# Kernel tuning notes

Hardware: AMD Instinct MI355X
Metric: run time of the kernel (lower is better)

## Reference

```python
import jax, jax.numpy as jnp
import numpy as np

B, C, H, W = 16, 512, 64, 64
HEADS = 8
DIL = 2  # dilation of the 3x3 depthwise conv (padding == dilation -> shape preserving)


def setup_inputs() -> dict:
    key = jax.random.key(0)
    ks = jax.random.split(key, 4)
    x = jax.random.normal(ks[0], (B, C, H, W), jnp.float32)
    # kaiming-normal-ish scales (fan_out, relu)
    w_qkv = jax.random.normal(ks[1], (3 * C, C), jnp.float32) * (2.0 / C) ** 0.5  # 1x1 conv weight
    w_dw = jax.random.normal(ks[2], (C, 3, 3), jnp.float32) * (2.0 / 9.0) ** 0.5  # depthwise 3x3
    w_out = jax.random.normal(ks[3], (C, C), jnp.float32) * (2.0 / C) ** 0.5      # 1x1 conv weight
    temperature = jnp.sqrt(jnp.asarray(C // HEADS, jnp.float32))                  # init sqrt(dim_per_head)
    return {"x": x, "w_qkv": w_qkv, "w_dw": w_dw, "w_out": w_out, "temperature": temperature}


def _dw_conv(y, w_dw):
    # depthwise dilated 3x3 conv, padding=dilation -> same spatial size
    rhs = w_dw[:, None, :, :]  # [C,1,3,3]
    return jax.lax.conv_general_dilated(
        y, rhs, window_strides=(1, 1), padding=((DIL, DIL), (DIL, DIL)),
        rhs_dilation=(DIL, DIL), feature_group_count=y.shape[1],
        dimension_numbers=("NCHW", "OIHW", "NCHW"))


def reference(x, w_qkv, w_dw, w_out, temperature):
    b, c, h, w = x.shape
    n = h * w
    d = c // HEADS
    # 1x1 qkv projection (bias-free conv == einsum)
    qkv = jnp.einsum("oc,bchw->bohw", w_qkv, x)  # [B,3C,H,W]
    q, k, v = jnp.split(qkv, 3, axis=1)
    # same depthwise conv applied to q,k,v: fold into batch, conv once
    qkv3 = _dw_conv(jnp.concatenate([q, k, v], axis=0), w_dw)  # [3B,C,H,W]
    q, k, v = jnp.split(qkv3, 3, axis=0)
    q = q.reshape(b, HEADS, d, n)
    k = k.reshape(b, HEADS, d, n)
    v = v.reshape(b, HEADS, d, n)
    # L2 normalize along the per-head channel dim (dim=2), eps=1e-12 like F.normalize
    l2 = lambda t: t / jnp.maximum(jnp.linalg.norm(t, axis=2, keepdims=True), 1e-12)
    q = l2(q)
    k = l2(k)
    # cross-covariance attention: [B,heads,d,d]
    attn = jnp.einsum("bhdn,bhen->bhde", q, k) / jnp.maximum(temperature, 1e-5)
    attn = jax.nn.softmax(attn, axis=-1)
    # dropout is identity in eval mode
    out = jnp.einsum("bhde,bhen->bhdn", attn, v).reshape(b, c, h, w)
    return jnp.einsum("oc,bchw->bohw", w_out, out)
```

## Files before the change

### kernel.cpp

```cpp
#include <hip/hip_runtime.h>

typedef __attribute__((ext_vector_type(8))) short bf16x8;
typedef __attribute__((ext_vector_type(8))) unsigned short ushort8;
typedef __attribute__((ext_vector_type(4))) float f32x4;
typedef __attribute__((ext_vector_type(2))) float f32x2;
typedef __attribute__((ext_vector_type(4))) unsigned int u32x4;
typedef __attribute__((ext_vector_type(2))) unsigned int u32x2;

__device__ __forceinline__ float bf2f(unsigned short u) {
  union { unsigned int i; float f; } v; v.i = ((unsigned int)u) << 16; return v.f;
}
__device__ __forceinline__ float asf(unsigned int u) {
  union { unsigned int i; float f; } v; v.i = u; return v.f;
}
__device__ __forceinline__ unsigned short f2bf(float f) {
  union { float f; unsigned int i; } v; v.f = f;
  unsigned int u = v.i;
  return (unsigned short)((u + 0x7FFFu + ((u >> 16) & 1u)) >> 16);
}
__device__ __forceinline__ void gload16(const void* g, void* l) {
  __builtin_amdgcn_global_load_lds(
      (const __attribute__((address_space(1))) void*)g,
      (__attribute__((address_space(3))) void*)l, 16, 0, 0);
}

__global__ __launch_bounds__(256) void cvt_f32_bf16(const float* __restrict__ s,
                                                    unsigned short* __restrict__ d, int n) {
  int i = blockIdx.x * 256 + threadIdx.x;
  if (i < n) d[i] = f2bf(s[i]);
}

__global__ __launch_bounds__(256) void transpose_x(const float* __restrict__ x,
                                                   unsigned short* __restrict__ xt) {
  __shared__ float tile[64][65];
  const int b = blockIdx.z, ct = blockIdx.y, nt = blockIdx.x;
  const int t = threadIdx.x;
  const int r0 = t >> 6, col = t & 63;
  const float* src = x + ((size_t)b * 512 + ct * 64) * 4096 + nt * 64;
#pragma unroll
  for (int i = 0; i < 16; ++i) {
    int r = i * 4 + r0;
    tile[r][col] = src[(size_t)r * 4096 + col];
  }
  __syncthreads();
  unsigned short* dst = xt + ((size_t)b * 4096 + nt * 64) * 512 + ct * 64;
  const int c2 = (t & 31) * 2;
  const int nsub = t >> 5;
#pragma unroll
  for (int i = 0; i < 8; ++i) {
    int n = i * 8 + nsub;
    unsigned int p;
    asm("v_cvt_pk_bf16_f32 %0, %1, %2" : "=v"(p) : "v"(tile[c2][n]), "v"(tile[c2 + 1][n]));
    *(unsigned int*)(dst + (size_t)n * 512 + c2) = p;
  }
}

template <bool BF16OUT>
__global__ __launch_bounds__(512, 1) void gemm256_8ph(const unsigned short* __restrict__ A,
                                                      const unsigned short* __restrict__ B,
                                                      void* __restrict__ Cv, int ldc,
                                                      size_t sA, size_t sB, size_t sC) {
  __shared__ unsigned short lA[2][256 * 64];
  __shared__ unsigned short lB[2][256 * 64];
  const int gx = gridDim.x, gy = gridDim.y;
  const int nwg = gx * gy * gridDim.z;
  int flat = blockIdx.x + gx * (blockIdx.y + gy * blockIdx.z);
  flat = (flat & 7) * (nwg >> 3) + (flat >> 3);
  const int bx = flat % gx;
  const int rem = flat / gx;
  const int by = rem % gy;
  const int bz = rem / gy;
  const size_t m0 = (size_t)by * 256;
  const size_t n0 = (size_t)bx * 256;
  A += (size_t)bz * sA;
  B += (size_t)bz * sB;

  const int t = threadIdx.x;
  const int lane = t & 63;
  const int wid = t >> 6;
  const int wm = wid >> 2, wn = wid & 3;
  const int ro = lane & 15, kq = lane >> 4;

  const int srow = t >> 3;
  const int sslot = t & 7;
  const int kslot = sslot ^ (srow & 7);

  auto stageA = [&](int kt, int h, int bbuf) {
    char* d = (char*)(&lA[bbuf][0]) + ((h * 128 + srow) * 64 + sslot * 8) * 2;
    const unsigned short* g = A + (m0 + h * 128 + srow) * 512 + kt * 64 + kslot * 8;
    gload16(g, d);
    gload16(g + (size_t)64 * 512, d + 64 * 128);
  };
  auto stageB = [&](int kt, int h, int bbuf) {
    char* d = (char*)(&lB[bbuf][0]) + ((h * 128 + srow) * 64 + sslot * 8) * 2;
    const unsigned short* g = B + (n0 + h * 128 + srow) * 512 + kt * 64 + kslot * 8;
    gload16(g, d);
    gload16(g + (size_t)64 * 512, d + 64 * 128);
  };

  f32x4 acc[8][4] = {};

  stageA(0, 0, 0); stageA(0, 1, 0);
  stageB(0, 0, 0); stageB(0, 1, 0);
  stageA(1, 0, 1); stageA(1, 1, 1);
  asm volatile("s_waitcnt vmcnt(4)" ::: "memory");
  __builtin_amdgcn_s_barrier();

#pragma unroll 1
  for (int kt = 0; kt < 8; ++kt) {
    const int c = kt & 1;
    const unsigned short* pa = &lA[c][0];
    const unsigned short* pb = &lB[c][0];
    const int slot0 = kq ^ (ro & 7);
    const int slot1 = (4 + kq) ^ (ro & 7);

    bf16x8 a0[8], a1[8], b0, b1, b2, b3;
#pragma unroll
    for (int i = 0; i < 8; ++i)
      a0[i] = *(const bf16x8*)&pa[(wm * 128 + i * 16 + ro) * 64 + slot0 * 8];
    b0 = *(const bf16x8*)&pb[(wn * 64 + 0 * 16 + ro) * 64 + slot0 * 8];
    b1 = *(const bf16x8*)&pb[(wn * 64 + 1 * 16 + ro) * 64 + slot0 * 8];
    if (kt + 1 < 8) stageB(kt + 1, 0, c ^ 1);
    asm volatile("" ::: "memory");
    __builtin_amdgcn_s_barrier();
    asm volatile("s_waitcnt lgkmcnt(0)" ::: "memory");
    __builtin_amdgcn_s_setprio(1);
#pragma unroll
    for (int i = 0; i < 8; ++i) {
      acc[i][0] = __builtin_amdgcn_mfma_f32_16x16x32_bf16(a0[i], b0, acc[i][0], 0, 0, 0);
      acc[i][1] = __builtin_amdgcn_mfma_f32_16x16x32_bf16(a0[i], b1, acc[i][1], 0, 0, 0);
    }
    __builtin_amdgcn_s_setprio(0);

    b2 = *(const bf16x8*)&pb[(wn * 64 + 2 * 16 + ro) * 64 + slot0 * 8];
    b3 = *(const bf16x8*)&pb[(wn * 64 + 3 * 16 + ro) * 64 + slot0 * 8];
    if (kt + 1 < 8) stageB(kt + 1, 1, c ^ 1);
    asm volatile("" ::: "memory");
    __builtin_amdgcn_s_barrier();
    asm volatile("s_waitcnt lgkmcnt(0)" ::: "memory");
    __builtin_amdgcn_s_setprio(1);
#pragma unroll
    for (int i = 0; i < 8; ++i) {
      acc[i][2] = __builtin_amdgcn_mfma_f32_16x16x32_bf16(a0[i], b2, acc[i][2], 0, 0, 0);
      acc[i][3] = __builtin_amdgcn_mfma_f32_16x16x32_bf16(a0[i], b3, acc[i][3], 0, 0, 0);
    }
    __builtin_amdgcn_s_setprio(0);

#pragma unroll
    for (int i = 0; i < 8; ++i)
      a1[i] = *(const bf16x8*)&pa[(wm * 128 + i * 16 + ro) * 64 + slot1 * 8];
    b0 = *(const bf16x8*)&pb[(wn * 64 + 0 * 16 + ro) * 64 + slot1 * 8];
    b1 = *(const bf16x8*)&pb[(wn * 64 + 1 * 16 + ro) * 64 + slot1 * 8];
    asm volatile("s_waitcnt lgkmcnt(0)" ::: "memory");
    __builtin_amdgcn_s_barrier();
    __builtin_amdgcn_s_setprio(1);
#pragma unroll
    for (int i = 0; i < 8; ++i) {
      acc[i][0] = __builtin_amdgcn_mfma_f32_16x16x32_bf16(a1[i], b0, acc[i][0], 0, 0, 0);
      acc[i][1] = __builtin_amdgcn_mfma_f32_16x16x32_bf16(a1[i], b1, acc[i][1], 0, 0, 0);
    }
    __builtin_amdgcn_s_setprio(0);

    b2 = *(const bf16x8*)&pb[(wn * 64 + 2 * 16 + ro) * 64 + slot1 * 8];
    b3 = *(const bf16x8*)&pb[(wn * 64 + 3 * 16 + ro) * 64 + slot1 * 8];
    if (kt + 2 < 8) { stageA(kt + 2, 0, c); stageA(kt + 2, 1, c); }
    asm volatile("s_waitcnt lgkmcnt(0)" ::: "memory");
    if (kt < 6)       asm volatile("s_waitcnt vmcnt(4)" ::: "memory");
    else if (kt == 6) asm volatile("s_waitcnt vmcnt(0)" ::: "memory");
    __builtin_amdgcn_s_barrier();
    __builtin_amdgcn_s_setprio(1);
#pragma unroll
    for (int i = 0; i < 8; ++i) {
      acc[i][2] = __builtin_amdgcn_mfma_f32_16x16x32_bf16(a1[i], b2, acc[i][2], 0, 0, 0);
      acc[i][3] = __builtin_amdgcn_mfma_f32_16x16x32_bf16(a1[i], b3, acc[i][3], 0, 0, 0);
    }
    __builtin_amdgcn_s_setprio(0);
  }

  if constexpr (BF16OUT) {
    unsigned short* C = (unsigned short*)Cv;
#pragma unroll
    for (int i = 0; i < 8; ++i)
#pragma unroll
      for (int j = 0; j < 4; ++j)
#pragma unroll
        for (int r = 0; r < 4; ++r) {
          size_t row = m0 + wm * 128 + i * 16 + (kq << 2) + r;
          size_t col = n0 + wn * 64 + j * 16 + ro;
          C[row * (size_t)ldc + col] = f2bf(acc[i][j][r]);
        }
  } else {
    float* C = (float*)Cv + (size_t)bz * sC;
#pragma unroll
    for (int i = 0; i < 8; ++i)
#pragma unroll
      for (int j = 0; j < 4; ++j)
#pragma unroll
        for (int r = 0; r < 4; ++r) {
          size_t row = m0 + wm * 128 + i * 16 + (kq << 2) + r;
          size_t col = n0 + wn * 64 + j * 16 + ro;
          C[row * (size_t)ldc + col] = acc[i][j][r];
        }
  }
}

struct Row4 { u32x2 v[4]; };

__global__ __launch_bounds__(256) void dwconv_norm(const unsigned short* __restrict__ Y,
                                                   const float* __restrict__ wdw,
                                                   unsigned short* __restrict__ Qb,
                                                   unsigned short* __restrict__ Kb,
                                                   unsigned short* __restrict__ Vb) {
  const int t = threadIdx.x, lane = t & 63, wv = t >> 6;
  const int bid = blockIdx.x;
  const int lbid = (bid & 7) * 384 + (bid >> 3);
  const int wid = lbid * 4 + wv;
  const int sub = wid & 255;
  const int grp = wid >> 8;
  const int pair = sub >> 3;
  const int par = (sub >> 2) & 1, chhalf = (sub >> 1) & 1, rowhalf = sub & 1;
  const int b = grp / 3, part = grp - b * 3;
  const int x0 = (pair >> 1) * 4 + (pair & 1);
  const int c0 = chhalf * 256 + (lane >> 4) * 64 + (lane & 15) * 4;

  f32x2 wa[9], wb[9];
  {
    float qw[36];
    const float* wp = wdw + c0 * 9;
#pragma unroll
    for (int i = 0; i < 9; ++i) {
      f32x4 q = *(const f32x4*)(wp + i * 4);
      qw[i * 4 + 0] = q[0]; qw[i * 4 + 1] = q[1];
      qw[i * 4 + 2] = q[2]; qw[i * 4 + 3] = q[3];
    }
#pragma unroll
    for (int tap = 0; tap < 9; ++tap) {
      wa[tap] = (f32x2){qw[tap], qw[9 + tap]};
      wb[tap] = (f32x2){qw[18 + tap], qw[27 + tap]};
    }
  }

  const size_t ybase = (size_t)b * 4096 * 1536 + part * 512 + c0;
  const bool okm = (x0 >= 2), okp = (x0 + 4 <= 63);
  const int cm = okm ? x0 - 2 : x0;
  const int cp = okp ? x0 + 4 : x0;

  auto loadrow = [&](int yy) -> Row4 {
    Row4 r;
    const bool oky = ((unsigned)yy < 64u);
    const int yyc = oky ? yy : 0;
    const size_t rb = ybase + (size_t)(yyc * 64) * 1536;
    u32x2 a = *(const u32x2*)(Y + rb + (size_t)cm * 1536);
    u32x2 c = *(const u32x2*)(Y + rb + (size_t)x0 * 1536);
    u32x2 d = *(const u32x2*)(Y + rb + (size_t)(x0 + 2) * 1536);
    u32x2 e = *(const u32x2*)(Y + rb + (size_t)cp * 1536);
    r.v[0] = a & ((oky && okm) ? 0xFFFFFFFFu : 0u);
    r.v[1] = c & (oky ? 0xFFFFFFFFu : 0u);
    r.v[2] = d & (oky ? 0xFFFFFFFFu : 0u);
    r.v[3] = e & ((oky && okp) ? 0xFFFFFFFFu : 0u);
    return r;
  };

  const int y0 = par + rowhalf * 32;
  Row4 W[3];
  W[0] = loadrow(y0 - 2);
  W[1] = loadrow(y0);
  W[2] = loadrow(y0 + 2);

  unsigned short* dstA = (part == 0 ? Qb : (part == 1 ? Kb : Vb)) +
                         ((size_t)b * 4096 + x0) * 512 + c0;
  unsigned short* dstB = dstA + (size_t)2 * 512;

#pragma unroll
  for (int i = 0; i < 16; ++i) {
    const int y = y0 + 2 * i;
    f32x2 A01 = (f32x2){0.f, 0.f}, A23 = (f32x2){0.f, 0.f};
    f32x2 B01 = (f32x2){0.f, 0.f}, B23 = (f32x2){0.f, 0.f};
#pragma unroll
    for (int r = 0; r < 3; ++r) {
      const Row4& R = W[(i + r) % 3];
#pragma unroll
      for (int xt = 0; xt < 4; ++xt) {
        const u32x2 v = R.v[xt];
        f32x2 lo = (f32x2){asf(v[0] << 16), asf(v[0] & 0xFFFF0000u)};
        f32x2 hi = (f32x2){asf(v[1] << 16), asf(v[1] & 0xFFFF0000u)};
        if (xt < 3) {
          const int tap = r * 3 + xt;
          A01 += lo * wa[tap];
          A23 += hi * wb[tap];
        }
        if (xt >= 1) {
          const int tap = r * 3 + xt - 1;
          B01 += lo * wa[tap];
          B23 += hi * wb[tap];
        }
      }
    }
    if (part < 2) {
      f32x2 sa = A01 * A01 + A23 * A23;
      f32x2 sb = B01 * B01 + B23 * B23;
      float ssa = sa[0] + sa[1];
      float ssb = sb[0] + sb[1];
#pragma unroll
      for (int m = 1; m <= 8; m <<= 1) {
        ssa += __shfl_xor(ssa, m);
        ssb += __shfl_xor(ssb, m);
      }
      const float ra = 1.f / fmaxf(sqrtf(ssa), 1e-12f);
      const float rb2 = 1.f / fmaxf(sqrtf(ssb), 1e-12f);
      A01 *= ra; A23 *= ra;
      B01 *= rb2; B23 *= rb2;
    }
    unsigned int p0, p1, q0, q1;
    asm("v_cvt_pk_bf16_f32 %0, %1, %2" : "=v"(p0) : "v"(A01[0]), "v"(A01[1]));
    asm("v_cvt_pk_bf16_f32 %0, %1, %2" : "=v"(p1) : "v"(A23[0]), "v"(A23[1]));
    asm("v_cvt_pk_bf16_f32 %0, %1, %2" : "=v"(q0) : "v"(B01[0]), "v"(B01[1]));
    asm("v_cvt_pk_bf16_f32 %0, %1, %2" : "=v"(q1) : "v"(B23[0]), "v"(B23[1]));
    u32x2 pkA; pkA[0] = p0; pkA[1] = p1;
    u32x2 pkB; pkB[0] = q0; pkB[1] = q1;
    *(u32x2*)(dstA + (size_t)y * 64 * 512) = pkA;
    *(u32x2*)(dstB + (size_t)y * 64 * 512) = pkB;
    if (i < 15) W[i % 3] = loadrow(y + 4);
  }
}

__global__ __launch_bounds__(256) void attn_partial(const unsigned short* __restrict__ Qb,
                                                    const unsigned short* __restrict__ Kb,
                                                    float* __restrict__ Spart) {
  __shared__ unsigned short sQ[4][64][72];
  __shared__ unsigned short sK[4][64][72];
  const int t = threadIdx.x, lane = t & 63, wv = t >> 6;
  const int bh = blockIdx.x >> 2;
  const int s = (blockIdx.x & 3) * 4 + wv;
  const int b = bh >> 3, h = bh & 7;
  const unsigned short* qbase = Qb + ((size_t)b * 4096) * 512 + h * 64;
  const unsigned short* kbase = Kb + ((size_t)b * 4096) * 512 + h * 64;
  f32x4 acc[4][4] = {};
  for (int ch = 0; ch < 4; ++ch) {
    const int n0 = s * 256 + ch * 64;
    const unsigned short* qp = qbase + (size_t)(n0 + lane) * 512;
    const unsigned short* kp = kbase + (size_t)(n0 + lane) * 512;
    ushort8 qv[8], kv[8];
#pragma unroll
    for (int v = 0; v < 8; ++v) qv[v] = *(const ushort8*)(qp + v * 8);
#pragma unroll
    for (int v = 0; v < 8; ++v) kv[v] = *(const ushort8*)(kp + v * 8);
#pragma unroll
    for (int v = 0; v < 8; ++v)
#pragma unroll
      for (int j = 0; j < 8; ++j) {
        sQ[wv][v * 8 + j][lane] = qv[v][j];
        sK[wv][v * 8 + j][lane] = kv[v][j];
      }
    __syncthreads();
    const int ro = lane & 15, ko = (lane >> 4) * 8;
#pragma unroll
    for (int ks = 0; ks < 2; ++ks) {
      bf16x8 af[4], bv[4];
#pragma unroll
      for (int i = 0; i < 4; ++i) af[i] = *(const bf16x8*)&sQ[wv][i * 16 + ro][ks * 32 + ko];
#pragma unroll
      for (int i = 0; i < 4; ++i) bv[i] = *(const bf16x8*)&sK[wv][i * 16 + ro][ks * 32 + ko];
#pragma unroll
      for (int i = 0; i < 4; ++i)
#pragma unroll
        for (int j = 0; j < 4; ++j)
          acc[i][j] = __builtin_amdgcn_mfma_f32_16x16x32_bf16(af[i], bv[j], acc[i][j], 0, 0, 0);
    }
    __syncthreads();
  }
  float* dst = Spart + ((size_t)bh * 16 + s) * 4096;
#pragma unroll
  for (int i = 0; i < 4; ++i)
#pragma unroll
    for (int j = 0; j < 4; ++j)
#pragma unroll
      for (int r = 0; r < 4; ++r) {
        int d = i * 16 + ((lane >> 4) << 2) + r;
        int e = j * 16 + (lane & 15);
        dst[d * 64 + e] = acc[i][j][r];
      }
}

__global__ __launch_bounds__(256) void softmax_attn(const float* __restrict__ Spart,
                                                    const float* __restrict__ tptr,
                                                    unsigned short* __restrict__ attn) {
  const int bh = blockIdx.x, t = threadIdx.x;
  const int d = t >> 2, eb = (t & 3) << 4;
  const float inv_t = 1.f / fmaxf(tptr[0], 1e-5f);
  float v[16];
#pragma unroll
  for (int i = 0; i < 16; ++i) v[i] = 0.f;
  for (int s = 0; s < 16; ++s) {
    const f32x4* p = (const f32x4*)(Spart + ((size_t)bh * 16 + s) * 4096 + d * 64 + eb);
#pragma unroll
    for (int i = 0; i < 4; ++i) {
      f32x4 q = p[i];
      v[i * 4 + 0] += q[0]; v[i * 4 + 1] += q[1];
      v[i * 4 + 2] += q[2]; v[i * 4 + 3] += q[3];
    }
  }
  float mx = -1e30f;
#pragma unroll
  for (int i = 0; i < 16; ++i) { v[i] *= inv_t; mx = fmaxf(mx, v[i]); }
  mx = fmaxf(mx, __shfl_xor(mx, 1));
  mx = fmaxf(mx, __shfl_xor(mx, 2));
  float sm = 0.f;
#pragma unroll
  for (int i = 0; i < 16; ++i) { v[i] = __expf(v[i] - mx); sm += v[i]; }
  sm += __shfl_xor(sm, 1);
  sm += __shfl_xor(sm, 2);
  const float r = 1.f / sm;
  ushort8 pk0, pk1;
#pragma unroll
  for (int i = 0; i < 8; ++i) { pk0[i] = f2bf(v[i] * r); pk1[i] = f2bf(v[8 + i] * r); }
  ushort8* dst = (ushort8*)(attn + (size_t)bh * 4096 + d * 64 + eb);
  dst[0] = pk0; dst[1] = pk1;
}

__global__ __launch_bounds__(256) void make_w2(const unsigned short* __restrict__ attn,
                                               const float* __restrict__ w_out,
                                               unsigned short* __restrict__ w2) {
  __shared__ float sA[4096];
  const int bx = blockIdx.x;
  const int bh = bx >> 1, half = bx & 1;
  const int b = bh >> 3, h = bh & 7;
  const int t = threadIdx.x;
  for (int i = t; i < 4096; i += 256) sA[i] = bf2f(attn[(size_t)bh * 4096 + i]);
  __syncthreads();
  const int o = half * 256 + t;
  float w[64];
  const float* wp = w_out + (size_t)o * 512 + h * 64;
#pragma unroll
  for (int i = 0; i < 64; i += 4) {
    f32x4 q = *(const f32x4*)(wp + i);
    w[i] = q[0]; w[i + 1] = q[1]; w[i + 2] = q[2]; w[i + 3] = q[3];
  }
  unsigned short* dst = w2 + ((size_t)b * 512 + o) * 512 + h * 64;
#pragma unroll 1
  for (int eg = 0; eg < 8; ++eg) {
    ushort8 pk;
#pragma unroll
    for (int ee = 0; ee < 8; ++ee) {
      const int e = eg * 8 + ee;
      float acc = 0.f;
#pragma unroll
      for (int dd = 0; dd < 64; ++dd) acc += w[dd] * sA[dd * 64 + e];
      pk[ee] = f2bf(acc);
    }
    *(ushort8*)(dst + eg * 8) = pk;
  }
}

extern "C" void kernel_launch(void* const* d_in, const int* in_sizes, int n_in,
                              void* d_out, int out_size, void* d_ws, size_t ws_size,
                              hipStream_t stream) {
  const float* x     = (const float*)d_in[0];
  const float* w_qkv = (const float*)d_in[1];
  const float* w_dw  = (const float*)d_in[2];
  const float* w_out = (const float*)d_in[3];
  const float* temp  = (const float*)d_in[4];
  float* out = (float*)d_out;

  char* ws = (char*)d_ws;
  const size_t MB = 1024 * 1024;
  unsigned short* Xt    = (unsigned short*)(ws);
  float*          Spart = (float*)(ws);
  unsigned short* attn  = (unsigned short*)(ws + 32 * MB);
  unsigned short* w2    = (unsigned short*)(ws + 33 * MB);
  unsigned short* Y     = (unsigned short*)(ws + 64 * MB);
  unsigned short* Qb    = (unsigned short*)(ws + 256 * MB);
  unsigned short* Kb    = (unsigned short*)(ws + 320 * MB);
  unsigned short* Vb    = (unsigned short*)(ws + 384 * MB);
  unsigned short* Wq    = (unsigned short*)(ws + 448 * MB);

  cvt_f32_bf16<<<3072, 256, 0, stream>>>(w_qkv, Wq, 1536 * 512);
  transpose_x<<<dim3(64, 8, 16), 256, 0, stream>>>(x, Xt);
  gemm256_8ph<true><<<dim3(6, 256, 1), 512, 0, stream>>>(Xt, Wq, Y, 1536, 0, 0, 0);
  dwconv_norm<<<3072, 256, 0, stream>>>(Y, w_dw, Qb, Kb, Vb);
  attn_partial<<<512, 256, 0, stream>>>(Qb, Kb, Spart);
  softmax_attn<<<128, 256, 0, stream>>>(Spart, temp, attn);
  make_w2<<<256, 256, 0, stream>>>(attn, w_out, w2);
  gemm256_8ph<false><<<dim3(16, 2, 16), 512, 0, stream>>>(
      w2, Vb, out, 4096,
      (size_t)512 * 512, (size_t)4096 * 512, (size_t)512 * 4096);
}
```

Measured before the change: 402.6 us.

## Use dedicated 128x128 tile GEMM kernel for QKV projection

Replaces the generic 256x256 eight-phase GEMM for the QKV projection with a specialized 128x128 tile kernel that uses 256 threads, two blocks per CU, double-buffered LDS with an XOR swizzle, and a hard-coded K of 512. The aim is more workgroups (6144 instead of 1536) for better CU occupancy and load balance, and more latency hiding through two resident blocks. In exchange each tile does less operand reuse, so more global and LDS traffic is spent per FLOP. The epilogue stores scalar bf16 values, which may make writes less efficient.

```diff
diff --git a/kernel.cpp b/kernel.cpp
--- a/kernel.cpp
+++ b/kernel.cpp
@@ -53,6 +53,105 @@
     asm("v_cvt_pk_bf16_f32 %0, %1, %2" : "=v"(p) : "v"(tile[c2][n]), "v"(tile[c2 + 1][n]));
     *(unsigned int*)(dst + (size_t)n * 512 + c2) = p;
   }
+}
+
+__global__ __launch_bounds__(256, 2) void gemm_qkv_128(const unsigned short* __restrict__ A,
+                                                       const unsigned short* __restrict__ B,
+                                                       unsigned short* __restrict__ C) {
+  __shared__ unsigned short lA[2][128 * 64];
+  __shared__ unsigned short lB[2][128 * 64];
+  const int gx = gridDim.x;
+  const int nwg = gx * gridDim.y;
+  int flat = blockIdx.x + gx * blockIdx.y;
+  flat = (flat & 7) * (nwg >> 3) + (flat >> 3);
+  const int bx = flat % gx;
+  const int by = flat / gx;
+  const size_t m0 = (size_t)by * 128;
+  const size_t n0 = (size_t)bx * 128;
+
+  const int t = threadIdx.x;
+  const int lane = t & 63;
+  const int wid = t >> 6;
+  const int wm = wid >> 1, wn = wid & 1;
+  const int ro = lane & 15, kq = lane >> 4;
+
+  const int srow = t >> 3;
+  const int sslot = t & 7;
+
+  auto stage = [&](int kt, int bbuf) {
+#pragma unroll
+    for (int l = 0; l < 4; ++l) {
+      const int row = l * 32 + srow;
+      const int kslot = sslot ^ (row & 7);
+      char* da = (char*)(&lA[bbuf][0]) + row * 128 + sslot * 16;
+      char* db = (char*)(&lB[bbuf][0]) + row * 128 + sslot * 16;
+      gload16(A + (m0 + row) * 512 + kt * 64 + kslot * 8, da);
+      gload16(B + (n0 + row) * 512 + kt * 64 + kslot * 8, db);
+    }
+  };
+
+  f32x4 acc[4][4] = {};
+
+  stage(0, 0);
+  stage(1, 1);
+  asm volatile("s_waitcnt vmcnt(8)" ::: "memory");
+  __builtin_amdgcn_s_barrier();
+
+#pragma unroll 1
+  for (int kt = 0; kt < 8; ++kt) {
+    const int c = kt & 1;
+    const unsigned short* pa = &lA[c][0];
+    const unsigned short* pb = &lB[c][0];
+    const int slot0 = kq ^ (ro & 7);
+    const int slot1 = (4 + kq) ^ (ro & 7);
+
+    bf16x8 a0[4], b0[4], a1[4], b1[4];
+#pragma unroll
+    for (int i = 0; i < 4; ++i)
+      a0[i] = *(const bf16x8*)&pa[(wm * 64 + i * 16 + ro) * 64 + slot0 * 8];
+#pragma unroll
+    for (int j = 0; j < 4; ++j)
+      b0[j] = *(const bf16x8*)&pb[(wn * 64 + j * 16 + ro) * 64 + slot0 * 8];
+    asm volatile("" ::: "memory");
+    __builtin_amdgcn_s_barrier();
+    asm volatile("s_waitcnt lgkmcnt(0)" ::: "memory");
+    __builtin_amdgcn_s_setprio(1);
+#pragma unroll
+    for (int i = 0; i < 4; ++i)
+#pragma unroll
+      for (int j = 0; j < 4; ++j)
+        acc[i][j] = __builtin_amdgcn_mfma_f32_16x16x32_bf16(a0[i], b0[j], acc[i][j], 0, 0, 0);
+    __builtin_amdgcn_s_setprio(0);
+
+#pragma unroll
+    for (int i = 0; i < 4; ++i)
+      a1[i] = *(const bf16x8*)&pa[(wm * 64 + i * 16 + ro) * 64 + slot1 * 8];
+#pragma unroll
+    for (int j = 0; j < 4; ++j)
+      b1[j] = *(const bf16x8*)&pb[(wn * 64 + j * 16 + ro) * 64 + slot1 * 8];
+    asm volatile("s_waitcnt lgkmcnt(0)" ::: "memory");
+    if (kt < 7) asm volatile("s_waitcnt vmcnt(0)" ::: "memory");
+    __builtin_amdgcn_s_barrier();
+    if (kt + 2 < 8) stage(kt + 2, c);
+    __builtin_amdgcn_s_setprio(1);
+#pragma unroll
+    for (int i = 0; i < 4; ++i)
+#pragma unroll
+      for (int j = 0; j < 4; ++j)
+        acc[i][j] = __builtin_amdgcn_mfma_f32_16x16x32_bf16(a1[i], b1[j], acc[i][j], 0, 0, 0);
+    __builtin_amdgcn_s_setprio(0);
+  }
+
+#pragma unroll
+  for (int i = 0; i < 4; ++i)
+#pragma unroll
+    for (int j = 0; j < 4; ++j)
+#pragma unroll
+      for (int r = 0; r < 4; ++r) {
+        size_t row = m0 + wm * 64 + i * 16 + (kq << 2) + r;
+        size_t col = n0 + wn * 64 + j * 16 + ro;
+        C[row * 1536 + col] = f2bf(acc[i][j][r]);
+      }
 }
 
 template <bool BF16OUT>
@@ -476,7 +575,7 @@
 
   cvt_f32_bf16<<<3072, 256, 0, stream>>>(w_qkv, Wq, 1536 * 512);
   transpose_x<<<dim3(64, 8, 16), 256, 0, stream>>>(x, Xt);
-  gemm256_8ph<true><<<dim3(6, 256, 1), 512, 0, stream>>>(Xt, Wq, Y, 1536, 0, 0, 0);
+  gemm_qkv_128<<<dim3(12, 512), 256, 0, stream>>>(Xt, Wq, Y);
   dwconv_norm<<<3072, 256, 0, stream>>>(Y, w_dw, Qb, Kb, Vb);
   attn_partial<<<512, 256, 0, stream>>>(Qb, Kb, Spart);
   softmax_attn<<<128, 256, 0, stream>>>(Spart, temp, attn);
```

Result: slower. 414.9 us (+3.1%).

## Use persistent QKV GEMM that sweeps all six N tiles per row block

Applied to the files above, without the earlier changes.

Replaces the 6x256-block QKV projection GEMM with a 256-block kernel where each workgroup owns one 256-row M tile and loops over all six 256-column N tiles. K and N tiles are pipelined continuously through double-buffered LDS, with an epilogue storing bf16 output every eight K steps. This is meant to remove the per-tile prologue and epilogue and to let the A tile stay hot in L2 across its N tiles. It launches one block per CU-sized slot, so load balance depends on having enough CUs, and the inline stores inside the main loop may stall the pipeline.

```diff
diff --git a/kernel.cpp b/kernel.cpp
--- a/kernel.cpp
+++ b/kernel.cpp
@@ -52,6 +52,140 @@
     unsigned int p;
     asm("v_cvt_pk_bf16_f32 %0, %1, %2" : "=v"(p) : "v"(tile[c2][n]), "v"(tile[c2 + 1][n]));
     *(unsigned int*)(dst + (size_t)n * 512 + c2) = p;
+  }
+}
+
+__global__ __launch_bounds__(512, 1) void gemm_qkv_pers(const unsigned short* __restrict__ A,
+                                                        const unsigned short* __restrict__ B,
+                                                        unsigned short* __restrict__ C) {
+  __shared__ unsigned short lA[2][256 * 64];
+  __shared__ unsigned short lB[2][256 * 64];
+  const int bid = blockIdx.x;
+  const int by = (bid & 7) * 32 + (bid >> 3);
+  const size_t m0 = (size_t)by * 256;
+
+  const int t = threadIdx.x;
+  const int lane = t & 63;
+  const int wid = t >> 6;
+  const int wm = wid >> 2, wn = wid & 3;
+  const int ro = lane & 15, kq = lane >> 4;
+
+  const int srow = t >> 3;
+  const int sslot = t & 7;
+  const int kslot = sslot ^ (srow & 7);
+
+  auto stageA = [&](int Tt, int h, int bbuf) {
+    const int kt = Tt & 7;
+    char* d = (char*)(&lA[bbuf][0]) + ((h * 128 + srow) * 64 + sslot * 8) * 2;
+    const unsigned short* g = A + (m0 + h * 128 + srow) * 512 + kt * 64 + kslot * 8;
+    gload16(g, d);
+    gload16(g + (size_t)64 * 512, d + 64 * 128);
+  };
+  auto stageB = [&](int Tt, int h, int bbuf) {
+    const int kt = Tt & 7;
+    const size_t nb = (size_t)(Tt >> 3) * 256;
+    char* d = (char*)(&lB[bbuf][0]) + ((h * 128 + srow) * 64 + sslot * 8) * 2;
+    const unsigned short* g = B + (nb + h * 128 + srow) * 512 + kt * 64 + kslot * 8;
+    gload16(g, d);
+    gload16(g + (size_t)64 * 512, d + 64 * 128);
+  };
+
+  f32x4 acc[8][4] = {};
+
+  stageA(0, 0, 0); stageA(0, 1, 0);
+  stageB(0, 0, 0); stageB(0, 1, 0);
+  stageA(1, 0, 1); stageA(1, 1, 1);
+  asm volatile("s_waitcnt vmcnt(4)" ::: "memory");
+  __builtin_amdgcn_s_barrier();
+
+#pragma unroll 1
+  for (int T = 0; T < 48; ++T) {
+    const int c = T & 1;
+    const unsigned short* pa = &lA[c][0];
+    const unsigned short* pb = &lB[c][0];
+    const int slot0 = kq ^ (ro & 7);
+    const int slot1 = (4 + kq) ^ (ro & 7);
+
+    bf16x8 a0[8], a1[8], b0, b1, b2, b3;
+#pragma unroll
+    for (int i = 0; i < 8; ++i)
+      a0[i] = *(const bf16x8*)&pa[(wm * 128 + i * 16 + ro) * 64 + slot0 * 8];
+    b0 = *(const bf16x8*)&pb[(wn * 64 + 0 * 16 + ro) * 64 + slot0 * 8];
+    b1 = *(const bf16x8*)&pb[(wn * 64 + 1 * 16 + ro) * 64 + slot0 * 8];
+    if (T + 1 < 48) stageB(T + 1, 0, c ^ 1);
+    asm volatile("" ::: "memory");
+    __builtin_amdgcn_s_barrier();
+    asm volatile("s_waitcnt lgkmcnt(0)" ::: "memory");
+    __builtin_amdgcn_s_setprio(1);
+#pragma unroll
+    for (int i = 0; i < 8; ++i) {
+      acc[i][0] = __builtin_amdgcn_mfma_f32_16x16x32_bf16(a0[i], b0, acc[i][0], 0, 0, 0);
+      acc[i][1] = __builtin_amdgcn_mfma_f32_16x16x32_bf16(a0[i], b1, acc[i][1], 0, 0, 0);
+    }
+    __builtin_amdgcn_s_setprio(0);
+
+    b2 = *(const bf16x8*)&pb[(wn * 64 + 2 * 16 + ro) * 64 + slot0 * 8];
+    b3 = *(const bf16x8*)&pb[(wn * 64 + 3 * 16 + ro) * 64 + slot0 * 8];
+    if (T + 1 < 48) stageB(T + 1, 1, c ^ 1);
+    asm volatile("" ::: "memory");
+    __builtin_amdgcn_s_barrier();
+    asm volatile("s_waitcnt lgkmcnt(0)" ::: "memory");
+    __builtin_amdgcn_s_setprio(1);
+#pragma unroll
+    for (int i = 0; i < 8; ++i) {
+      acc[i][2] = __builtin_amdgcn_mfma_f32_16x16x32_bf16(a0[i], b2, acc[i][2], 0, 0, 0);
+      acc[i][3] = __builtin_amdgcn_mfma_f32_16x16x32_bf16(a0[i], b3, acc[i][3], 0, 0, 0);
+    }
+    __builtin_amdgcn_s_setprio(0);
+
+#pragma unroll
+    for (int i = 0; i < 8; ++i)
+      a1[i] = *(const bf16x8*)&pa[(wm * 128 + i * 16 + ro) * 64 + slot1 * 8];
+    b0 = *(const bf16x8*)&pb[(wn * 64 + 0 * 16 + ro) * 64 + slot1 * 8];
+    b1 = *(const bf16x8*)&pb[(wn * 64 + 1 * 16 + ro) * 64 + slot1 * 8];
+    asm volatile("s_waitcnt lgkmcnt(0)" ::: "memory");
+    __builtin_amdgcn_s_barrier();
+    __builtin_amdgcn_s_setprio(1);
+#pragma unroll
+    for (int i = 0; i < 8; ++i) {
+      acc[i][0] = __builtin_amdgcn_mfma_f32_16x16x32_bf16(a1[i], b0, acc[i][0], 0, 0, 0);
+      acc[i][1] = __builtin_amdgcn_mfma_f32_16x16x32_bf16(a1[i], b1, acc[i][1], 0, 0, 0);
+    }
+    __builtin_amdgcn_s_setprio(0);
+
+    b2 = *(const bf16x8*)&pb[(wn * 64 + 2 * 16 + ro) * 64 + slot1 * 8];
+    b3 = *(const bf16x8*)&pb[(wn * 64 + 3 * 16 + ro) * 64 + slot1 * 8];
+    if (T + 2 < 48) { stageA(T + 2, 0, c); stageA(T + 2, 1, c); }
+    asm volatile("s_waitcnt lgkmcnt(0)" ::: "memory");
+    if (T < 46)       asm volatile("s_waitcnt vmcnt(4)" ::: "memory");
+    else if (T == 46) asm volatile("s_waitcnt vmcnt(0)" ::: "memory");
+    __builtin_amdgcn_s_barrier();
+    __builtin_amdgcn_s_setprio(1);
+#pragma unroll
+    for (int i = 0; i < 8; ++i) {
+      acc[i][2] = __builtin_amdgcn_mfma_f32_16x16x32_bf16(a1[i], b2, acc[i][2], 0, 0, 0);
+      acc[i][3] = __builtin_amdgcn_mfma_f32_16x16x32_bf16(a1[i], b3, acc[i][3], 0, 0, 0);
+    }
+    __builtin_amdgcn_s_setprio(0);
+
+    if ((T & 7) == 7) {
+      const size_t cb = (size_t)(T >> 3) * 256;
+#pragma unroll
+      for (int i = 0; i < 8; ++i)
+#pragma unroll
+        for (int j = 0; j < 4; ++j)
+#pragma unroll
+          for (int r = 0; r < 4; ++r) {
+            size_t row = m0 + wm * 128 + i * 16 + (kq << 2) + r;
+            size_t col = cb + wn * 64 + j * 16 + ro;
+            C[row * 1536 + col] = f2bf(acc[i][j][r]);
+          }
+#pragma unroll
+      for (int i = 0; i < 8; ++i)
+#pragma unroll
+        for (int j = 0; j < 4; ++j)
+          acc[i][j] = (f32x4){0.f, 0.f, 0.f, 0.f};
+    }
   }
 }
 
@@ -476,7 +610,7 @@
 
   cvt_f32_bf16<<<3072, 256, 0, stream>>>(w_qkv, Wq, 1536 * 512);
   transpose_x<<<dim3(64, 8, 16), 256, 0, stream>>>(x, Xt);
-  gemm256_8ph<true><<<dim3(6, 256, 1), 512, 0, stream>>>(Xt, Wq, Y, 1536, 0, 0, 0);
+  gemm_qkv_pers<<<256, 512, 0, stream>>>(Xt, Wq, Y);
   dwconv_norm<<<3072, 256, 0, stream>>>(Y, w_dw, Qb, Kb, Vb);
   attn_partial<<<512, 256, 0, stream>>>(Qb, Kb, Spart);
   softmax_attn<<<128, 256, 0, stream>>>(Spart, temp, attn);
```

Result: slower. 440.8 us (+9.5%).
